# Performance work log

Measured on AMD Instinct MI355X. Metric: run time of the kernel, lower is better.

The kernel has to match this reference:

```python
import jax, jax.numpy as jnp
import numpy as np

IN_FEATURES = 4096
OUT_FEATURES = 4096
R = 4                       # number of diagonal blocks
BLK = IN_FEATURES // R      # 1024, size of each Cayley block
EPS = 1e-5


def setup_inputs() -> dict:
    key = jax.random.key(0)
    k1, k2, k3 = jax.random.split(key, 3)
    x = jax.random.normal(k1, (8, 1024, IN_FEATURES), dtype=jnp.float32)
    # oft_R is initialized to zeros in the module; use small random values so
    # the COFT projection / Cayley transform are numerically non-trivial.
    oft_R = jax.random.normal(k2, (R, BLK, BLK), dtype=jnp.float32) * 0.01
    weight = jax.random.normal(k3, (OUT_FEATURES, IN_FEATURES), dtype=jnp.float32) * 0.02
    return {"x": x, "oft_R": oft_R, "weight": weight}


def _project_batch(Rm, eps):
    # torch project_batch: I is ZEROS (not identity), so diff == R.
    eps = eps / jnp.sqrt(jnp.asarray(Rm.shape[0], Rm.dtype))
    norm = jnp.linalg.norm(Rm.reshape(Rm.shape[0], -1), axis=1).reshape(-1, 1, 1)
    return jnp.where(norm <= eps, Rm, eps * Rm / norm)


def _cayley_batch(Rm):
    # Q = (I - skew) @ inv(I + skew), skew = 0.5 * (R - R^T)
    skew = 0.5 * (Rm - jnp.swapaxes(Rm, 1, 2))
    I = jnp.eye(Rm.shape[1], dtype=Rm.dtype)
    return jnp.matmul(I - skew, jnp.linalg.inv(I + skew))


def reference(x, oft_R, weight):
    eps = EPS * BLK * BLK  # self.eps in the module
    # COFT projection happens under no_grad via copy_: straight-through.
    R_proj = oft_R + jax.lax.stop_gradient(_project_batch(oft_R, eps) - oft_R)
    Q = _cayley_batch(R_proj)                      # (R, BLK, BLK) orthogonal blocks
    # torch uses weight.data -> detached from autograd.
    W = jax.lax.stop_gradient(weight)
    # block_diag(Q) @ W^T, done block-wise (same math, no zero-padded matrix).
    Wt_blocks = W.T.reshape(R, BLK, OUT_FEATURES)  # (R, BLK, OUT)
    filt_t = jnp.einsum('rij,rjo->rio', Q, Wt_blocks).reshape(IN_FEATURES, OUT_FEATURES)
    # F.linear(x, filt) with filt = filt_t^T  ->  x @ filt_t
    return jnp.matmul(x, filt_t)
```

## Files before the change

kernel.cpp:

```cpp
#include <hip/hip_runtime.h>
#include <cstdint>


typedef __attribute__((ext_vector_type(4))) float facc4;
typedef __attribute__((ext_vector_type(8))) short bfrag8;

__device__ __forceinline__ unsigned short f2bf(float x) {
  union { float f; unsigned int u; } v; v.f = x;
  unsigned int r = v.u + 0x7fffu + ((v.u >> 16) & 1u);
  return (unsigned short)(r >> 16);
}

__device__ __forceinline__ float bf2f(unsigned short b) {
  union { unsigned int u; float f; } v; v.u = ((unsigned int)b) << 16;
  return v.f;
}

__device__ __forceinline__ void gload16(const void* g, void* lds) {
  __builtin_amdgcn_global_load_lds(
      (__attribute__((address_space(1))) void*)(uintptr_t)g,
      (__attribute__((address_space(3))) void*)(uintptr_t)(uint32_t)(uintptr_t)lds,
      16, 0, 0);
}

__device__ __forceinline__ void bar() {
  __builtin_amdgcn_s_barrier();
}


__global__ void norm_partials(const float* __restrict__ R, float* __restrict__ part) {
  int r = blockIdx.y, seg = blockIdx.x;
  const float* base = R + (long)r * 1048576 + (long)seg * 16384;
  float s = 0.f;
  for (int i = threadIdx.x; i < 4096; i += 256) {
    float4 v = ((const float4*)base)[i];
    s += v.x * v.x + v.y * v.y + v.z * v.z + v.w * v.w;
  }
  __shared__ float red[256];
  red[threadIdx.x] = s;
  __syncthreads();
  for (int off = 128; off; off >>= 1) {
    if (threadIdx.x < off) red[threadIdx.x] += red[threadIdx.x + off];
    __syncthreads();
  }
  if (threadIdx.x == 0) part[r * 64 + seg] = red[0];
}

__global__ void finalize_scale(const float* __restrict__ part, float* __restrict__ scale) {
  int r = blockIdx.x;
  float s = part[r * 64 + threadIdx.x];
  for (int off = 32; off; off >>= 1) s += __shfl_down(s, off);
  if (threadIdx.x == 0) {
    float norm = sqrtf(s);
    const float eps = 5.24288f;
    scale[r] = (norm <= eps) ? 1.f : eps / norm;
  }
}

__global__ void build_S(const float* __restrict__ R, const float* __restrict__ scale,
                        unsigned short* __restrict__ S) {
  int r = blockIdx.z;
  float c = 0.5f * scale[r];
  const float* Rb = R + (long)r * 1048576;
  unsigned short* Sb = S + (long)r * 1048576;
  int bi = blockIdx.x, bj = blockIdx.y;
  int tx = threadIdx.x, ty = threadIdx.y;
  __shared__ float tbuf[32][33];
  for (int yy = ty; yy < 32; yy += 8)
    tbuf[yy][tx] = Rb[(long)(bj * 32 + yy) * 1024 + bi * 32 + tx];
  __syncthreads();
  for (int yy = ty; yy < 32; yy += 8) {
    int i = bi * 32 + yy, j = bj * 32 + tx;
    float s = c * (Rb[(long)i * 1024 + j] - tbuf[tx][yy]);
    Sb[(long)i * 1024 + j] = f2bf(s);
  }
}

__device__ void gemm_q_body(int bx, int by, int bz,
                            const unsigned short* __restrict__ A,
                            const unsigned short* __restrict__ B,
                            const unsigned short* __restrict__ E,
                            unsigned short* __restrict__ C) {
  __shared__ __align__(16) unsigned short As[4096];
  __shared__ __align__(16) unsigned short Bs[4096];
  const long LD = 1024, STR = 1048576;
  const int t = threadIdx.x;
  const int l = t & 63;
  const int w = t >> 6;
  const long m0 = (long)bx * 128;
  const long n0 = (long)by * 128;
  A += (long)bz * STR;
  B += (long)bz * STR;
  E += (long)bz * STR;
  C += (long)bz * STR;

  const int srow = t >> 2;
  const int scol = (t & 3) * 8;
  const unsigned short* gA0 = A + (m0 + srow) * LD + scol;
  const unsigned short* gA1 = A + (m0 + srow + 64) * LD + scol;
  const unsigned short* gB0 = B + (n0 + srow) * LD + scol;
  const unsigned short* gB1 = B + (n0 + srow + 64) * LD + scol;

  facc4 acc[4][4];
#pragma unroll
  for (int i = 0; i < 4; ++i)
#pragma unroll
    for (int j = 0; j < 4; ++j) acc[i][j] = (facc4){0.f, 0.f, 0.f, 0.f};

  const int wr = (w >> 1) * 64;
  const int wc = (w & 1) * 64;
  const int fr = l & 15;
  const int kg = (l >> 4) * 8;

  for (int k0 = 0; k0 < 1024; k0 += 32) {
    __syncthreads();
    gload16(gA0 + k0, &As[t * 8]);
    gload16(gA1 + k0, &As[t * 8 + 2048]);
    gload16(gB0 + k0, &Bs[t * 8]);
    gload16(gB1 + k0, &Bs[t * 8 + 2048]);
    __syncthreads();
    bfrag8 af[4], bfr[4];
#pragma unroll
    for (int mf = 0; mf < 4; ++mf)
      af[mf] = *(const bfrag8*)&As[(wr + mf * 16 + fr) * 32 + kg];
#pragma unroll
    for (int nf = 0; nf < 4; ++nf)
      bfr[nf] = *(const bfrag8*)&Bs[(wc + nf * 16 + fr) * 32 + kg];
#pragma unroll
    for (int mf = 0; mf < 4; ++mf)
#pragma unroll
      for (int nf = 0; nf < 4; ++nf)
        acc[mf][nf] = __builtin_amdgcn_mfma_f32_16x16x32_bf16(
            af[mf], bfr[nf], acc[mf][nf], 0, 0, 0);
  }

  const int orow = (l >> 4) * 4;
#pragma unroll
  for (int mf = 0; mf < 4; ++mf) {
#pragma unroll
    for (int nf = 0; nf < 4; ++nf) {
#pragma unroll
      for (int r = 0; r < 4; ++r) {
        long grow = m0 + wr + mf * 16 + orow + r;
        long gcol = n0 + wc + nf * 16 + fr;
        float d = (grow == gcol) ? 1.f : 0.f;
        float sv = bf2f(E[grow * LD + gcol]);
        float v = d - 2.f * sv - 2.f * acc[mf][nf][r];
        C[grow * LD + gcol] = f2bf(v);
      }
    }
  }
}

__global__ __launch_bounds__(256) void fused_prep(
    const unsigned short* __restrict__ S, unsigned short* __restrict__ Q,
    const float* __restrict__ x, unsigned short* __restrict__ Xb,
    const float* __restrict__ W, unsigned short* __restrict__ Wb) {
  const int b = blockIdx.x;
  if (b < 256) {
    gemm_q_body(b & 7, (b >> 3) & 7, b >> 6, S, S, S, Q);
  } else if (b < 1024) {
    const long stride = 768L * 256;
    for (long i = (long)(b - 256) * 256 + threadIdx.x; i < 8388608; i += stride) {
      float4 v = ((const float4*)x)[i];
      ushort4 o;
      o.x = f2bf(v.x); o.y = f2bf(v.y); o.z = f2bf(v.z); o.w = f2bf(v.w);
      ((ushort4*)Xb)[i] = o;
    }
  } else {
    const long stride = 384L * 256;
    for (long i = (long)(b - 1024) * 256 + threadIdx.x; i < 4194304; i += stride) {
      float4 v = ((const float4*)W)[i];
      ushort4 o;
      o.x = f2bf(v.x); o.y = f2bf(v.y); o.z = f2bf(v.z); o.w = f2bf(v.w);
      ((ushort4*)Wb)[i] = o;
    }
  }
}

#define AC_(db, h) (((db) * 2 + (h)) * 8192)
#define BC_(db, h) (32768 + ((db) * 2 + (h)) * 8192)

template <int F32OUT>
__global__ __launch_bounds__(512, 2) void gemm256(
    const unsigned short* __restrict__ A, long lda, long sA,
    const unsigned short* __restrict__ B, long ldb, long sB,
    void* __restrict__ C, long ldc, long sC, int K,
    int cm, int cn, int ncm) {
  __shared__ __align__(16) unsigned short Lsh[65536];
  const int t = threadIdx.x;
  const int l = t & 63;
  const int wid = t >> 6;
  const int wr = wid >> 2;
  const int wc = wid & 3;
  const int fr = l & 15;
  const int lk = l >> 4;
  const int z = blockIdx.z;
  const unsigned short* Ab = A + (long)z * sA;
  const unsigned short* Bb = B + (long)z * sB;

  const int wg = blockIdx.x;
  const int xcd = wg & 7;
  const int j = wg >> 3;
  const long m0 = (long)((xcd % ncm) * cm + (j % cm)) * 256;
  const long n0 = (long)((xcd / ncm) * cn + (j / cm)) * 256;

  const int r0 = t >> 3, r1 = 64 + (t >> 3);
  const int kg0 = (t & 7) ^ (r0 & 7);
  const int kg1 = (t & 7) ^ (r1 & 7);
  const long soA0 = (long)r0 * lda + kg0 * 8;
  const long soA1 = (long)r1 * lda + kg1 * 8;
  const long soB0 = (long)r0 * ldb + kg0 * 8;
  const long soB1 = (long)r1 * ldb + kg1 * 8;
  const int ldo0 = t * 8, ldo1 = (512 + t) * 8;

  const unsigned short* gA0_ = Ab + m0 * lda;
  const unsigned short* gA1_ = Ab + (m0 + 128) * lda;
  const unsigned short* gB0_ = Bb + n0 * ldb;
  const unsigned short* gB1_ = Bb + (n0 + 128) * ldb;

#define STG_A(h, kt, cb) do { \
    const unsigned short* _g = (h) ? gA1_ : gA0_; \
    gload16(_g + soA0 + (long)(kt) * 64, &Lsh[(cb) + ldo0]); \
    gload16(_g + soA1 + (long)(kt) * 64, &Lsh[(cb) + ldo1]); } while (0)
#define STG_B(h, kt, cb) do { \
    const unsigned short* _g = (h) ? gB1_ : gB0_; \
    gload16(_g + soB0 + (long)(kt) * 64, &Lsh[(cb) + ldo0]); \
    gload16(_g + soB1 + (long)(kt) * 64, &Lsh[(cb) + ldo1]); } while (0)

  const int xk0 = (lk ^ (fr & 7)) * 8;
  const int xk1 = ((4 + lk) ^ (fr & 7)) * 8;
  const int rB = (wc & 1) * 64;

  facc4 acc[8][4];
#pragma unroll
  for (int i = 0; i < 8; ++i)
#pragma unroll
    for (int j2 = 0; j2 < 4; ++j2) acc[i][j2] = (facc4){0.f, 0.f, 0.f, 0.f};
  bfrag8 aL[4][2], aH[4][2], bl[2][2], bh[2][2];

#define MMQ(MO, NO, AF, BF) do { \
    __builtin_amdgcn_s_setprio(1); \
    _Pragma("unroll") for (int kk = 0; kk < 2; ++kk) \
    _Pragma("unroll") for (int m = 0; m < 4; ++m) \
    _Pragma("unroll") for (int n = 0; n < 2; ++n) \
      acc[(MO) + m][(NO) + n] = __builtin_amdgcn_mfma_f32_16x16x32_bf16( \
          AF[m][kk], BF[n][kk], acc[(MO) + m][(NO) + n], 0, 0, 0); \
    __builtin_amdgcn_s_setprio(0); } while (0)

#define LGKM0 do { asm volatile("s_waitcnt lgkmcnt(0)"); \
                   __builtin_amdgcn_sched_barrier(0); } while (0)

#define TILE(DB, S_) do { \
    const int cAo = (DB) * 16384 + wr * 8192; \
    const int cBo = 32768 + (DB) * 16384 + (wc >> 1) * 8192; \
     \
    _Pragma("unroll") for (int m = 0; m < 4; ++m) { \
      int rb = cAo + (m * 16 + fr) * 64; \
      aL[m][0] = *(const bfrag8*)&Lsh[rb + xk0]; \
      aL[m][1] = *(const bfrag8*)&Lsh[rb + xk1]; \
    } \
    _Pragma("unroll") for (int n = 0; n < 2; ++n) { \
      int rb = cBo + (rB + n * 16 + fr) * 64; \
      bl[n][0] = *(const bfrag8*)&Lsh[rb + xk0]; \
      bl[n][1] = *(const bfrag8*)&Lsh[rb + xk1]; \
    } \
    if ((S_) + 1 < NT) STG_A(1, (S_) + 1, AC_((DB) ^ 1, 1)); \
    asm volatile("s_waitcnt lgkmcnt(8)"); \
    bar(); LGKM0; \
    MMQ(0, 0, aL, bl); \
    bar(); \
     \
    _Pragma("unroll") for (int n = 0; n < 2; ++n) { \
      int rb = cBo + (rB + 32 + n * 16 + fr) * 64; \
      bh[n][0] = *(const bfrag8*)&Lsh[rb + xk0]; \
      bh[n][1] = *(const bfrag8*)&Lsh[rb + xk1]; \
    } \
    bar(); LGKM0; \
    MMQ(0, 2, aL, bh); \
    bar(); \
     \
    _Pragma("unroll") for (int m = 0; m < 4; ++m) { \
      int rb = cAo + (64 + m * 16 + fr) * 64; \
      aH[m][0] = *(const bfrag8*)&Lsh[rb + xk0]; \
      aH[m][1] = *(const bfrag8*)&Lsh[rb + xk1]; \
    } \
    if ((S_) + 2 < NT) STG_B(0, (S_) + 2, BC_((DB), 0)); \
    bar(); LGKM0; \
    MMQ(4, 0, aH, bl); \
    bar(); \
     \
    if ((S_) + 2 < NT) { STG_A(0, (S_) + 2, AC_((DB), 0)); \
                         STG_B(1, (S_) + 2, BC_((DB), 1)); } \
    bar(); \
    MMQ(4, 2, aH, bh); \
    if ((S_) + 2 < NT) asm volatile("s_waitcnt vmcnt(6)"); \
    else               asm volatile("s_waitcnt vmcnt(0)"); \
    __builtin_amdgcn_sched_barrier(0); \
    bar(); \
  } while (0)

  STG_B(0, 0, BC_(0, 0));
  STG_A(0, 0, AC_(0, 0));
  STG_B(1, 0, BC_(0, 1));
  STG_A(1, 0, AC_(0, 1));
  STG_B(0, 1, BC_(1, 0));
  STG_A(0, 1, AC_(1, 0));
  STG_B(1, 1, BC_(1, 1));
  asm volatile("s_waitcnt vmcnt(6)");
  __builtin_amdgcn_sched_barrier(0);
  bar();

  const int NT = K >> 6;
  for (int s = 0; s < NT; s += 2) {
    TILE(0, s);
    TILE(1, s + 1);
  }

#pragma unroll
  for (int m = 0; m < 8; ++m) {
#pragma unroll
    for (int n = 0; n < 4; ++n) {
#pragma unroll
      for (int r = 0; r < 4; ++r) {
        long grow = m0 + wr * 128 + m * 16 + lk * 4 + r;
        long gcol = n0 + wc * 64 + n * 16 + fr;
        if (F32OUT) {
          ((float*)C + (long)z * sC)[grow * ldc + gcol] = acc[m][n][r];
        } else {
          ((unsigned short*)C + (long)z * sC)[grow * ldc + gcol] = f2bf(acc[m][n][r]);
        }
      }
    }
  }
#undef STG_A
#undef STG_B
#undef MMQ
#undef LGKM0
#undef TILE
}

static const size_t OFF_SCALE = 0;
static const size_t OFF_PART  = 1024;
static const size_t OFF_S     = 4ull << 20;
static const size_t OFF_PA    = 12ull << 20;
static const size_t OFF_W     = 28ull << 20;
static const size_t OFF_FILT  = 60ull << 20;
static const size_t OFF_XBF   = 92ull << 20;

extern "C" void kernel_launch(void* const* d_in, const int* in_sizes, int n_in,
                              void* d_out, int out_size, void* d_ws, size_t ws_size,
                              hipStream_t stream) {
  const float* x    = (const float*)d_in[0];
  const float* oftR = (const float*)d_in[1];
  const float* W    = (const float*)d_in[2];
  char* ws = (char*)d_ws;
  float* scale = (float*)(ws + OFF_SCALE);
  float* part  = (float*)(ws + OFF_PART);
  unsigned short* S  = (unsigned short*)(ws + OFF_S);
  unsigned short* Q  = (unsigned short*)(ws + OFF_PA);
  unsigned short* Wb = (unsigned short*)(ws + OFF_W);
  unsigned short* Fl = (unsigned short*)(ws + OFF_FILT);
  unsigned short* Xb = (unsigned short*)(ws + OFF_XBF);

  norm_partials<<<dim3(64, 4), 256, 0, stream>>>(oftR, part);
  finalize_scale<<<4, 64, 0, stream>>>(part, scale);
  build_S<<<dim3(32, 32, 4), dim3(32, 8), 0, stream>>>(oftR, scale, S);

  fused_prep<<<1408, 256, 0, stream>>>(S, Q, x, Xb, W, Wb);

  gemm256<0><<<dim3(64, 1, 4), 512, 0, stream>>>(
      Wb, 4096, 1024, Q, 1024, 1048576, Fl, 4096, 1024, 1024, 4, 2, 4);
  gemm256<1><<<dim3(512, 1, 1), 512, 0, stream>>>(
      Xb, 4096, 0, Fl, 4096, 0, d_out, 4096, 0, 4096, 8, 8, 4);
}
```

Measured before the change: 357.8 us.

## Move x bf16 conversion into the filter GEMM launch to overlap with compute

Measured after the change: 360.1 us. No clear change (+0.6%).

```diff
diff --git a/kernel.cpp b/kernel.cpp
--- a/kernel.cpp
+++ b/kernel.cpp
@@ -154,22 +154,13 @@
 
 __global__ __launch_bounds__(256) void fused_prep(
     const unsigned short* __restrict__ S, unsigned short* __restrict__ Q,
-    const float* __restrict__ x, unsigned short* __restrict__ Xb,
     const float* __restrict__ W, unsigned short* __restrict__ Wb) {
   const int b = blockIdx.x;
   if (b < 256) {
     gemm_q_body(b & 7, (b >> 3) & 7, b >> 6, S, S, S, Q);
-  } else if (b < 1024) {
-    const long stride = 768L * 256;
-    for (long i = (long)(b - 256) * 256 + threadIdx.x; i < 8388608; i += stride) {
-      float4 v = ((const float4*)x)[i];
-      ushort4 o;
-      o.x = f2bf(v.x); o.y = f2bf(v.y); o.z = f2bf(v.z); o.w = f2bf(v.w);
-      ((ushort4*)Xb)[i] = o;
-    }
   } else {
     const long stride = 384L * 256;
-    for (long i = (long)(b - 1024) * 256 + threadIdx.x; i < 4194304; i += stride) {
+    for (long i = (long)(b - 256) * 256 + threadIdx.x; i < 4194304; i += stride) {
       float4 v = ((const float4*)W)[i];
       ushort4 o;
       o.x = f2bf(v.x); o.y = f2bf(v.y); o.z = f2bf(v.z); o.w = f2bf(v.w);
@@ -182,12 +173,12 @@
 #define BC_(db, h) (32768 + ((db) * 2 + (h)) * 8192)
 
 template <int F32OUT>
-__global__ __launch_bounds__(512, 2) void gemm256(
+__device__ void gemm256_body(
+    unsigned short* __restrict__ Lsh, int wg, int z,
     const unsigned short* __restrict__ A, long lda, long sA,
     const unsigned short* __restrict__ B, long ldb, long sB,
     void* __restrict__ C, long ldc, long sC, int K,
     int cm, int cn, int ncm) {
-  __shared__ __align__(16) unsigned short Lsh[65536];
   const int t = threadIdx.x;
   const int l = t & 63;
   const int wid = t >> 6;
@@ -195,11 +186,9 @@
   const int wc = wid & 3;
   const int fr = l & 15;
   const int lk = l >> 4;
-  const int z = blockIdx.z;
   const unsigned short* Ab = A + (long)z * sA;
   const unsigned short* Bb = B + (long)z * sB;
 
-  const int wg = blockIdx.x;
   const int xcd = wg & 7;
   const int j = wg >> 3;
   const long m0 = (long)((xcd % ncm) * cm + (j % cm)) * 256;
@@ -340,6 +329,38 @@
 #undef TILE
 }
 
+__global__ __launch_bounds__(512, 2) void gemm256_out(
+    const unsigned short* __restrict__ A, long lda,
+    const unsigned short* __restrict__ B, long ldb,
+    float* __restrict__ C, long ldc, int K,
+    int cm, int cn, int ncm) {
+  __shared__ __align__(16) unsigned short Lsh[65536];
+  gemm256_body<1>(Lsh, blockIdx.x, 0, A, lda, 0, B, ldb, 0, C, ldc, 0, K,
+                  cm, cn, ncm);
+}
+
+__global__ __launch_bounds__(512, 2) void fused_filt(
+    const unsigned short* __restrict__ Wb,
+    const unsigned short* __restrict__ Q,
+    unsigned short* __restrict__ Fl,
+    const float* __restrict__ x, unsigned short* __restrict__ Xb) {
+  __shared__ __align__(16) unsigned short Lsh[65536];
+  const int b = blockIdx.x;
+  if (b < 256) {
+    gemm256_body<0>(Lsh, b & 63, b >> 6,
+                    Wb, 4096, 1024, Q, 1024, 1048576,
+                    Fl, 4096, 1024, 1024, 4, 2, 4);
+  } else {
+    const long stride = 768L * 512;
+    for (long i = (long)(b - 256) * 512 + threadIdx.x; i < 8388608; i += stride) {
+      float4 v = ((const float4*)x)[i];
+      ushort4 o;
+      o.x = f2bf(v.x); o.y = f2bf(v.y); o.z = f2bf(v.z); o.w = f2bf(v.w);
+      ((ushort4*)Xb)[i] = o;
+    }
+  }
+}
+
 static const size_t OFF_SCALE = 0;
 static const size_t OFF_PART  = 1024;
 static const size_t OFF_S     = 4ull << 20;
@@ -367,10 +388,10 @@
   finalize_scale<<<4, 64, 0, stream>>>(part, scale);
   build_S<<<dim3(32, 32, 4), dim3(32, 8), 0, stream>>>(oftR, scale, S);
 
-  fused_prep<<<1408, 256, 0, stream>>>(S, Q, x, Xb, W, Wb);
-
-  gemm256<0><<<dim3(64, 1, 4), 512, 0, stream>>>(
-      Wb, 4096, 1024, Q, 1024, 1048576, Fl, 4096, 1024, 1024, 4, 2, 4);
-  gemm256<1><<<dim3(512, 1, 1), 512, 0, stream>>>(
-      Xb, 4096, 0, Fl, 4096, 0, d_out, 4096, 0, 4096, 8, 8, 4);
-}
+  fused_prep<<<640, 256, 0, stream>>>(S, Q, W, Wb);
+
+  fused_filt<<<1024, 512, 0, stream>>>(Wb, Q, Fl, x, Xb);
+
+  gemm256_out<<<512, 512, 0, stream>>>(
+      Xb, 4096, Fl, 4096, (float*)d_out, 4096, 4096, 8, 8, 4);
+}
```
